# Optimization experiments

Hardware: AMD Instinct MI355X
Metric: run time of the kernel (lower is better)

Reference implementation:

```python
import jax, jax.numpy as jnp
import numpy as np

DIM = 128; DSTATE = 8; DCONV = 4; DTRANK = 8
B = 2; T = 48; H = 16; W = 16
EPS = 1e-5

def _ln(x, w, b):
    mu = jnp.mean(x, -1, keepdims=True)
    var = jnp.mean(jnp.square(x - mu), -1, keepdims=True)
    return (x - mu) * jax.lax.rsqrt(var + EPS) * w + b

def _causal_dwconv(x, w, b):
    # x: [B,L,D], w: [D,K] depthwise, causal padding K-1 on the left
    xt = jnp.transpose(x, (0, 2, 1))  # [B,D,L]
    out = jax.lax.conv_general_dilated(
        xt, w[:, None, :], (1,), [(w.shape[-1] - 1, 0)],
        dimension_numbers=('NCH', 'OIH', 'NCH'),
        feature_group_count=x.shape[-1])
    return jnp.transpose(out + b[:, None], (0, 2, 1))

def _selective_scan(u, dt, A, Bc, Cc, Dp):
    # u, dt: [B,L,D]; A: [D,N]; Bc, Cc: [B,L,N]; Dp: [D]
    dA = jnp.exp(dt[..., None] * A)                          # [B,L,D,N]
    dBx = dt[..., None] * Bc[:, :, None, :] * u[..., None]   # [B,L,D,N]
    def combine(c1, c2):
        a1, b1 = c1; a2, b2 = c2
        return a1 * a2, a2 * b1 + b2
    _, hs = jax.lax.associative_scan(combine, (dA, dBx), axis=1)
    return jnp.einsum('bldn,bln->bld', hs, Cc) + u * Dp

def _bimamba(xn, in_w, conv_w, conv_b, xp_w, dt_w, dt_b, A_log, Dp, out_w):
    # xn: [B,L,DIM]; direction-stacked params have leading axis 2 (fwd/bwd)
    xz = xn @ in_w.T                      # [B,L,2*DIM]
    xh, z = jnp.split(xz, 2, axis=-1)
    acc = 0.0
    for d in range(2):
        xi = xh if d == 0 else xh[:, ::-1]
        zi = z if d == 0 else z[:, ::-1]
        xc = jax.nn.silu(_causal_dwconv(xi, conv_w[d], conv_b[d]))
        proj = xc @ xp_w[d].T             # [B,L,DTRANK+2*DSTATE]
        dtr, Bc, Cc = jnp.split(proj, [DTRANK, DTRANK + DSTATE], axis=-1)
        dt = jax.nn.softplus(dtr @ dt_w[d].T + dt_b[d])
        A = -jnp.exp(A_log[d])
        y = _selective_scan(xc, dt, A, Bc, Cc, Dp[d]) * jax.nn.silu(zi)
        acc = acc + (y if d == 0 else y[:, ::-1])
    return acc @ out_w.T

def setup_inputs():
    key = jax.random.key(0)
    ks = jax.random.split(key, 10)
    s = 0.1
    return {
        "x": jax.random.normal(ks[0], (B, DIM, T, H, W), jnp.float32),
        "norm1_w": jnp.ones((DIM,), jnp.float32),
        "norm1_b": jnp.zeros((DIM,), jnp.float32),
        "norm2_w": jnp.ones((DIM,), jnp.float32),
        "norm2_b": jnp.zeros((DIM,), jnp.float32),
        "subln_w": jnp.ones((DIM,), jnp.float32),
        "subln_b": jnp.zeros((DIM,), jnp.float32),
        "lambda_q": jax.random.normal(ks[1], (DIM,), jnp.float32) * s,
        "in_proj_w": jax.random.normal(ks[2], (2, 2 * DIM, DIM), jnp.float32) * s,
        "conv_w": jax.random.normal(ks[3], (2, 2, DIM, DCONV), jnp.float32) * s,
        "conv_b": jax.random.normal(ks[4], (2, 2, DIM), jnp.float32) * s,
        "x_proj_w": jax.random.normal(ks[5], (2, 2, DTRANK + 2 * DSTATE, DIM), jnp.float32) * s,
        "dt_proj_w": jax.random.normal(ks[6], (2, 2, DIM, DTRANK), jnp.float32) * s,
        "dt_proj_b": jax.random.normal(ks[7], (2, 2, DIM), jnp.float32) * s,
        "A_log": jnp.broadcast_to(jnp.log(jnp.arange(1, DSTATE + 1, dtype=jnp.float32)), (2, 2, DIM, DSTATE)) + 0.0,
        "D": jnp.ones((2, 2, DIM), jnp.float32),
        "out_proj_w": jax.random.normal(ks[8], (2, DIM, DIM), jnp.float32) * s,
    }

def reference(x, norm1_w, norm1_b, norm2_w, norm2_b, subln_w, subln_b,
              lambda_q, in_proj_w, conv_w, conv_b, x_proj_w,
              dt_proj_w, dt_proj_b, A_log, D, out_proj_w):
    Bsz, C = x.shape[0], x.shape[1]
    Tt, Hh, Ww = x.shape[2], x.shape[3], x.shape[4]
    L = Tt * Hh * Ww
    x_flat = jnp.transpose(x.reshape(Bsz, C, L), (0, 2, 1))  # [B,L,C]
    x_norm = _ln(x_flat, norm1_w, norm1_b)
    y1 = _bimamba(x_norm, in_proj_w[0], conv_w[0], conv_b[0], x_proj_w[0],
                  dt_proj_w[0], dt_proj_b[0], A_log[0], D[0], out_proj_w[0])
    y2 = _bimamba(x_norm, in_proj_w[1], conv_w[1], conv_b[1], x_proj_w[1],
                  dt_proj_w[1], dt_proj_b[1], A_log[1], D[1], out_proj_w[1])
    lam = jax.nn.sigmoid(jnp.sum(lambda_q))
    attn = _ln(y1 - lam * y2, subln_w, subln_b)
    out = _ln(x_flat + attn, norm2_w, norm2_b)
    return jnp.transpose(out, (0, 2, 1)).reshape(Bsz, C, Tt, Hh, Ww)
```

## Files before the change

kernel.cpp:

```cpp
#include <hip/hip_runtime.h>
#include <math.h>

#define DIMC 128
#define LSEQ 12288
#define NB 2
#define BLR 24576
#define EPSV 1e-5f
#define NCH 384
#define LC 32
#define KP 132
#define FBP 20

typedef __bf16 bf16x8 __attribute__((ext_vector_type(8)));
typedef __attribute__((ext_vector_type(4))) float f4_t;

__device__ __forceinline__ float sigf(float x){ return 1.f/(1.f+__expf(-x)); }
__device__ __forceinline__ float softplusf(float x){
    return fmaxf(x,0.f) + __logf(1.f + __expf(-fabsf(x)));
}
__device__ __forceinline__ float bf2f(unsigned short u){
    union { unsigned int i; float f; } v; v.i = ((unsigned int)u) << 16; return v.f;
}
__device__ __forceinline__ unsigned short f2bf(float f){
    union { float f; unsigned int i; } v; v.f = f;
    unsigned int b = v.i + 0x7FFFu + ((v.i >> 16) & 1u);
    return (unsigned short)(b >> 16);
}
__device__ __forceinline__ bf16x8 ld_frag8(const unsigned short* p){
    union { uint2 u[2]; bf16x8 v; } r;
    r.u[0] = *(const uint2*)(p);
    r.u[1] = *(const uint2*)(p+4);
    return r.v;
}
__device__ __forceinline__ bf16x8 ld_frag16g(const unsigned short* p){
    union { uint4 u; bf16x8 v; } r; r.u = *(const uint4*)p; return r.v;
}

template<bool FAST>
__device__ __forceinline__ void comp_a8(float dtv, const float* Av, float* a){
    if (FAST){
        float e1 = __expf(dtv*Av[0]);
        float e2 = e1*e1, e4 = e2*e2;
        a[0]=e1; a[1]=e2; a[2]=e2*e1; a[3]=e4;
        a[4]=e4*e1; a[5]=e4*e2; a[6]=a[5]*e1; a[7]=e4*e4;
    } else {
        #pragma unroll
        for (int n = 0; n < 8; n++) a[n] = __expf(dtv*Av[n]);
    }
}

__global__ void k_wall(const float* __restrict__ dtw, const float* __restrict__ xpw,
                       const float* __restrict__ lq,
                       unsigned short* __restrict__ wallb, float* __restrict__ lam){
    int inst = blockIdx.x, j = blockIdx.y, k = threadIdx.x;
    const float* xp = xpw + (size_t)inst*24*128;
    float v;
    if (j < 128){
        const float* dw = dtw + (size_t)inst*128*8 + (size_t)j*8;
        v = 0.f;
        #pragma unroll
        for (int r = 0; r < 8; r++) v += dw[r]*xp[r*128 + k];
    } else {
        v = xp[(8 + (j-128))*128 + k];
    }
    wallb[((size_t)inst*144 + j)*128 + k] = f2bf(v);
    if (inst == 0 && j == 0 && k < 64){
        float s = lq[k] + lq[k+64];
        for (int m = 32; m; m >>= 1) s += __shfl_xor(s, m);
        if (k == 0) *lam = 1.f/(1.f+__expf(-s));
    }
}

__global__ __launch_bounds__(256) void k_prep(const float* __restrict__ wi, const float* __restrict__ ow,
    unsigned short* __restrict__ wib, unsigned short* __restrict__ owb){
    int idx = (blockIdx.x*256 + threadIdx.x)*4;
    const float* src; unsigned short* dst; int off;
    if (idx < 65536){ src = wi;  dst = wib; off = idx; }
    else            { src = ow;  dst = owb; off = idx - 65536; }
    float4 v = *(const float4*)&src[off];
    ushort4 o; o.x=f2bf(v.x); o.y=f2bf(v.y); o.z=f2bf(v.z); o.w=f2bf(v.w);
    *(ushort4*)&dst[off] = o;
}

__global__ __launch_bounds__(256) void k_normT(const float* __restrict__ x,
    const float* __restrict__ w1, const float* __restrict__ b1, unsigned short* __restrict__ xn)
{
    __shared__ float t[64*129];
    __shared__ float red1[256], red2[256];
    __shared__ float stt[128];
    const int bb = blockIdx.x / 192;
    const int l0 = (blockIdx.x % 192) * 64;
    const int tid = threadIdx.x;
    const int li = tid & 63, cg = tid >> 6;
    #pragma unroll
    for (int p = 0; p < 32; p++){
        int c = p*4 + cg;
        t[li*129 + c] = x[(size_t)bb*DIMC*LSEQ + (size_t)c*LSEQ + l0 + li];
    }
    __syncthreads();
    {
        int r = tid >> 2, qg = tid & 3;
        float s = 0.f, s2 = 0.f;
        #pragma unroll
        for (int j = 0; j < 32; j++){ float v = t[r*129 + qg*32 + j]; s += v; s2 += v*v; }
        red1[qg*64 + r] = s; red2[qg*64 + r] = s2;
    }
    __syncthreads();
    if (tid < 64){
        float s = 0.f, s2 = 0.f;
        #pragma unroll
        for (int g = 0; g < 4; g++){ s += red1[g*64 + tid]; s2 += red2[g*64 + tid]; }
        float mu = s*(1.f/128.f);
        float var = s2*(1.f/128.f) - mu*mu;
        stt[tid*2] = mu; stt[tid*2+1] = rsqrtf(var + EPSV);
    }
    __syncthreads();
    const int c2 = (tid & 63)*2, lg = tid >> 6;
    #pragma unroll
    for (int p = 0; p < 16; p++){
        int l = p*4 + lg;
        float mu = stt[l*2], rs = stt[l*2+1];
        float v0 = (t[l*129 + c2    ] - mu)*rs*w1[c2    ] + b1[c2    ];
        float v1 = (t[l*129 + c2 + 1] - mu)*rs*w1[c2 + 1] + b1[c2 + 1];
        unsigned int o = (unsigned int)f2bf(v0) | ((unsigned int)f2bf(v1) << 16);
        *(unsigned int*)&xn[(size_t)(bb*LSEQ + l0 + l)*DIMC + c2] = o;
    }
}

__global__ __launch_bounds__(256,4) void k_inproj(const unsigned short* __restrict__ xn,
    const unsigned short* __restrict__ wib, unsigned short* __restrict__ xz)
{
    __shared__ __align__(16) unsigned short As[64*KP];
    const int row0 = blockIdx.x * 64;
    const int j0   = blockIdx.y * 128;
    const int tid = threadIdx.x;
    const int lane = tid & 63, w = tid >> 6;
    const int m15 = lane & 15, q = lane >> 4;
    const unsigned short* wb = wib + ((size_t)j0 + m15)*DIMC + q*8;
    bf16x8 bc[8], bn[8];
    #pragma unroll
    for (int nt = 0; nt < 8; nt++) bc[nt] = ld_frag16g(wb + nt*2048);
    #pragma unroll
    for (int p = 0; p < 4; p++){
        int idx = p*256 + tid; int li = idx >> 4; int g = (idx & 15)*8;
        uint4 va = *(const uint4*)&xn[(size_t)(row0+li)*DIMC + g];
        *(uint2*)&As[li*KP + g]     = make_uint2(va.x, va.y);
        *(uint2*)&As[li*KP + g + 4] = make_uint2(va.z, va.w);
    }
    __syncthreads();
    f4_t zf = {0.f,0.f,0.f,0.f};
    f4_t acc[8];
    #pragma unroll
    for (int j = 0; j < 8; j++) acc[j] = zf;
    #pragma unroll
    for (int ks = 0; ks < 4; ks++){
        if (ks < 3){
            #pragma unroll
            for (int nt = 0; nt < 8; nt++) bn[nt] = ld_frag16g(wb + nt*2048 + (ks+1)*32);
        }
        bf16x8 a0 = ld_frag8(&As[(w*16 + m15)*KP + ks*32 + q*8]);
        #pragma unroll
        for (int nt = 0; nt < 8; nt++)
            acc[nt] = __builtin_amdgcn_mfma_f32_16x16x32_bf16(a0, bc[nt], acc[nt], 0,0,0);
        #pragma unroll
        for (int nt = 0; nt < 8; nt++) bc[nt] = bn[nt];
    }
    __syncthreads();
    unsigned short* ep = As;
    #pragma unroll
    for (int nt = 0; nt < 8; nt++){
        int row = w*16 + q*4;
        int col = nt*16 + m15;
        #pragma unroll
        for (int i = 0; i < 4; i++)
            ep[(row+i)*KP + col] = f2bf(acc[nt][i]);
    }
    __syncthreads();
    #pragma unroll
    for (int p = 0; p < 4; p++){
        int idx = p*256 + tid; int li = idx >> 4; int g = (idx & 15)*8;
        uint2 u0 = *(const uint2*)&ep[li*KP + g];
        uint2 u1 = *(const uint2*)&ep[li*KP + g + 4];
        uint4 o; o.x=u0.x; o.y=u0.y; o.z=u1.x; o.w=u1.y;
        *(uint4*)&xz[(size_t)(row0+li)*512 + j0 + g] = o;
    }
}

template<bool FAST>
__device__ __forceinline__ void fscan(const unsigned short* __restrict__ As,
    const unsigned short* __restrict__ Ep, const float* __restrict__ fbuf,
    const float* Av, int ch, int d, int dim, float* Ac, float* Bc)
{
    #pragma unroll 8
    for (int s = 0; s < LC; s++){
        int r = ch*32 + (d ? 31-s : s);
        float dtv = bf2f(Ep[r*KP + dim]);
        float uv  = bf2f(As[r*KP + dim]);
        float4 b0 = *(const float4*)&fbuf[r*FBP];
        float4 b1 = *(const float4*)&fbuf[r*FBP + 4];
        float bv[8] = {b0.x,b0.y,b0.z,b0.w,b1.x,b1.y,b1.z,b1.w};
        float du = dtv*uv;
        float a[8];
        comp_a8<FAST>(dtv, Av, a);
        #pragma unroll
        for (int n = 0; n < 8; n++){
            Bc[n] = a[n]*Bc[n] + du*bv[n];
            Ac[n] *= a[n];
        }
    }
}

__global__ __launch_bounds__(256,4) void k_xproj(const unsigned short* __restrict__ xz,
    const unsigned short* __restrict__ wallb, const float* __restrict__ dtb,
    const float* __restrict__ alog, const float* __restrict__ cw, const float* __restrict__ cbv,
    unsigned short* __restrict__ xc, unsigned short* __restrict__ dty,
    float* __restrict__ bcb, float* __restrict__ st)
{
    __shared__ __align__(16) unsigned short As[64*KP];
    __shared__ __align__(16) unsigned short Zb[67*KP];
    __shared__ __align__(16) float fbuf[64*FBP];
    const int row0 = blockIdx.x * 64;
    const int ib   = blockIdx.y;
    const int inst = ib >> 1;
    const int bb   = ib & 1;
    const int m    = inst >> 1;
    const int d    = inst & 1;
    const int tid = threadIdx.x;
    const size_t abase = (size_t)ib * LSEQ * DIMC;
    const int lane = tid & 63, w = tid >> 6;
    const int m15 = lane & 15, q = lane >> 4;
    const unsigned short* wb = wallb + ((size_t)inst*144 + m15)*DIMC + q*8;
    bf16x8 bc[9], bn[9];
    #pragma unroll
    for (int nt = 0; nt < 9; nt++) bc[nt] = ld_frag16g(wb + nt*2048);
    const int start = row0 - (d ? 0 : 3);
    for (int idx = tid; idx < 67*16; idx += 256){
        int r = idx >> 4, cq = idx & 15;
        int l = start + r;
        uint4 v = make_uint4(0,0,0,0);
        if (l >= 0 && l < LSEQ)
            v = *(const uint4*)&xz[((size_t)(bb*LSEQ + l))*512 + m*256 + cq*8];
        *(uint4*)&Zb[r*KP + cq*8] = v;
    }
    __syncthreads();
    {
        const int dimi = tid & 127, lg = tid >> 7;
        float wk[4];
        #pragma unroll
        for (int k = 0; k < 4; k++){
            int kk = d ? 3-k : k;
            wk[k] = cw[((size_t)inst*DIMC + dimi)*4 + kk];
        }
        const float bsv = cbv[inst*DIMC + dimi];
        for (int p = 0; p < 32; p++){
            int li = p*2 + lg;
            float t0 = bf2f(Zb[(li  )*KP + dimi]);
            float t1 = bf2f(Zb[(li+1)*KP + dimi]);
            float t2 = bf2f(Zb[(li+2)*KP + dimi]);
            float t3 = bf2f(Zb[(li+3)*KP + dimi]);
            float v = bsv + wk[0]*t0 + wk[1]*t1 + wk[2]*t2 + wk[3]*t3;
            v = v * sigf(v);
            unsigned short uo = f2bf(v);
            As[li*KP + dimi] = uo;
            xc[abase + (size_t)(row0+li)*DIMC + dimi] = uo;
        }
    }
    __syncthreads();
    f4_t zf = {0.f,0.f,0.f,0.f};
    f4_t acc[9];
    #pragma unroll
    for (int j = 0; j < 9; j++) acc[j] = zf;
    #pragma unroll
    for (int ks = 0; ks < 4; ks++){
        if (ks < 3){
            #pragma unroll
            for (int nt = 0; nt < 9; nt++) bn[nt] = ld_frag16g(wb + nt*2048 + (ks+1)*32);
        }
        bf16x8 a0 = ld_frag8(&As[(w*16 + m15)*KP + ks*32 + q*8]);
        #pragma unroll
        for (int nt = 0; nt < 9; nt++)
            acc[nt] = __builtin_amdgcn_mfma_f32_16x16x32_bf16(a0, bc[nt], acc[nt], 0,0,0);
        #pragma unroll
        for (int nt = 0; nt < 9; nt++) bc[nt] = bn[nt];
    }
    unsigned short* Ep = Zb;
    {
        int row = w*16 + q*4;
        #pragma unroll
        for (int i = 0; i < 4; i++)
            fbuf[(row+i)*FBP + m15] = acc[8][i];
    }
    #pragma unroll
    for (int nt = 0; nt < 8; nt++){
        int col = nt*16 + m15;
        float bias = dtb[inst*DIMC + col];
        int row = w*16 + q*4;
        #pragma unroll
        for (int i = 0; i < 4; i++)
            Ep[(row+i)*KP + col] = f2bf(softplusf(acc[nt][i] + bias));
    }
    __syncthreads();
    {
        int row = tid >> 2, j = (tid & 3)*4;
        float4 v = { fbuf[row*FBP + j], fbuf[row*FBP + j + 1],
                     fbuf[row*FBP + j + 2], fbuf[row*FBP + j + 3] };
        *(float4*)&bcb[((size_t)ib*LSEQ + row0 + row)*16 + j] = v;
    }
    #pragma unroll
    for (int p = 0; p < 4; p++){
        int idx = p*256 + tid; int li = idx >> 4; int g = (idx & 15)*8;
        uint2 u0 = *(const uint2*)&Ep[li*KP + g];
        uint2 u1 = *(const uint2*)&Ep[li*KP + g + 4];
        uint4 o; o.x=u0.x; o.y=u0.y; o.z=u1.x; o.w=u1.y;
        *(uint4*)&dty[abase + (size_t)(row0+li)*DIMC + g] = o;
    }
    const int ch  = tid >> 7;
    const int dim = tid & 127;
    const int bc2 = row0 >> 5;
    const int c   = d ? (NCH-1 - bc2 - ch) : (bc2 + ch);
    float Av[8];
    #pragma unroll
    for (int n = 0; n < 8; n++)
        Av[n] = -__expf(alog[((size_t)inst*DIMC + dim)*8 + n]);
    bool fast = true;
    #pragma unroll
    for (int n = 1; n < 8; n++)
        fast = fast && (fabsf(Av[n] - (float)(n+1)*Av[0]) <= 1e-5f*fabsf(Av[n]));
    float Ac[8], Bc[8];
    #pragma unroll
    for (int n = 0; n < 8; n++){ Ac[n] = 1.f; Bc[n] = 0.f; }
    if (fast) fscan<true >(As, Ep, fbuf, Av, ch, d, dim, Ac, Bc);
    else      fscan<false>(As, Ep, fbuf, Av, ch, d, dim, Ac, Bc);
    float* so = st + (((size_t)ib*NCH + c)*DIMC + dim)*16;
    float4 s0 = {Ac[0],Ac[1],Ac[2],Ac[3]};
    float4 s1 = {Ac[4],Ac[5],Ac[6],Ac[7]};
    float4 s2 = {Bc[0],Bc[1],Bc[2],Bc[3]};
    float4 s3 = {Bc[4],Bc[5],Bc[6],Bc[7]};
    *(float4*)&so[0]  = s0;
    *(float4*)&so[4]  = s1;
    *(float4*)&so[8]  = s2;
    *(float4*)&so[12] = s3;
}

__global__ __launch_bounds__(512) void k_scan2(float* __restrict__ st){
    const int ib   = blockIdx.x >> 7;
    const int dim  = blockIdx.x & 127;
    const int n    = threadIdx.x >> 6;
    const int lane = threadIdx.x & 63;
    const size_t cstride = (size_t)DIMC*16;
    const size_t base = ((size_t)ib*NCH*DIMC + dim)*16 + n;
    float a[6], b[6];
    float Al = 1.f, Bl = 0.f;
    #pragma unroll
    for (int j = 0; j < 6; j++){
        size_t o = base + (size_t)(lane*6 + j)*cstride;
        float A  = st[o];
        float Bv = st[o + 8];
        a[j] = A; b[j] = Bv;
        Bl = A*Bl + Bv;
        Al *= A;
    }
    #pragma unroll
    for (int off = 1; off < 64; off <<= 1){
        float Ao = __shfl_up(Al, off, 64);
        float Bo = __shfl_up(Bl, off, 64);
        if (lane >= off){
            Bl = Al*Bo + Bl;
            Al = Al*Ao;
        }
    }
    float h = __shfl_up(Bl, 1, 64);
    if (lane == 0) h = 0.f;
    #pragma unroll
    for (int j = 0; j < 6; j++){
        size_t o = base + (size_t)(lane*6 + j)*cstride;
        st[o] = h;
        h = a[j]*h + b[j];
    }
}

template<bool FAST>
__device__ __forceinline__ void scan3_body(unsigned short* __restrict__ dty,
    const unsigned short* __restrict__ sdt, const unsigned short* __restrict__ sxc,
    const unsigned short* __restrict__ sz, const float* __restrict__ sbc,
    const float* Av, float Dv, float* h,
    size_t rbase, size_t lbase, int d, int tid)
{
    #pragma unroll 8
    for (int s = 0; s < LC; s++){
        int r = d ? 31-s : s;
        float dtv = bf2f(sdt[r*128 + tid]);
        float uv  = bf2f(sxc[r*128 + tid]);
        float zv  = bf2f(sz [r*128 + tid]);
        float4 bA = *(const float4*)&sbc[r*16];
        float4 bB = *(const float4*)&sbc[r*16 + 4];
        float4 cA = *(const float4*)&sbc[r*16 + 8];
        float4 cB = *(const float4*)&sbc[r*16 + 12];
        float bv[8] = {bA.x,bA.y,bA.z,bA.w,bB.x,bB.y,bB.z,bB.w};
        float cv[8] = {cA.x,cA.y,cA.z,cA.w,cB.x,cB.y,cB.z,cB.w};
        float du = dtv*uv;
        float y = uv*Dv;
        float a[8];
        comp_a8<FAST>(dtv, Av, a);
        #pragma unroll
        for (int n = 0; n < 8; n++){
            h[n] = a[n]*h[n] + du*bv[n];
            y += h[n]*cv[n];
        }
        y *= zv * sigf(zv);
        dty[rbase + (lbase + r)*DIMC + tid] = f2bf(y);
    }
}

__global__ __launch_bounds__(128) void k_scan3(unsigned short* __restrict__ dty,
    const unsigned short* __restrict__ xc, const float* __restrict__ bcb,
    const unsigned short* __restrict__ xz, const float* __restrict__ st,
    const float* __restrict__ alog, const float* __restrict__ dvec)
{
    __shared__ __align__(16) unsigned short sdt[32*128];
    __shared__ __align__(16) unsigned short sxc[32*128];
    __shared__ __align__(16) unsigned short sz [32*128];
    __shared__ __align__(16) float sbc[32*16];
    const int ib = blockIdx.x & 7;
    const int c  = blockIdx.x >> 3;
    const int inst = ib >> 1, bb = ib & 1;
    const int m = inst >> 1, d = inst & 1;
    const int tid = threadIdx.x;
    const size_t rbase = (size_t)ib*LSEQ*DIMC;
    const size_t zbase = (size_t)bb*LSEQ*512 + m*256 + 128;
    const size_t lbase = d ? (size_t)(LSEQ - 32 - c*32) : (size_t)(c*32);
    #pragma unroll
    for (int p = 0; p < 4; p++){
        int idx = p*128 + tid;
        int r = idx >> 4, g = (idx & 15)*8;
        size_t go = rbase + (lbase + r)*DIMC + g;
        *(uint4*)&sdt[r*128 + g] = *(const uint4*)&dty[go];
        *(uint4*)&sxc[r*128 + g] = *(const uint4*)&xc[go];
        *(uint4*)&sz [r*128 + g] = *(const uint4*)&xz[zbase + (lbase + r)*512 + g];
    }
    {
        int r = tid >> 2, j = (tid & 3)*4;
        *(float4*)&sbc[r*16 + j] = *(const float4*)&bcb[((size_t)ib*LSEQ + lbase + r)*16 + j];
    }
    float Av[8];
    #pragma unroll
    for (int n = 0; n < 8; n++)
        Av[n] = -__expf(alog[((size_t)inst*DIMC + tid)*8 + n]);
    bool fast = true;
    #pragma unroll
    for (int n = 1; n < 8; n++)
        fast = fast && (fabsf(Av[n] - (float)(n+1)*Av[0]) <= 1e-5f*fabsf(Av[n]));
    const float Dv = dvec[inst*DIMC + tid];
    float h[8];
    const float* hp = st + (((size_t)ib*NCH + c)*DIMC + tid)*16;
    #pragma unroll
    for (int n = 0; n < 8; n++) h[n] = hp[n];
    __syncthreads();
    if (fast) scan3_body<true >(dty, sdt, sxc, sz, sbc, Av, Dv, h, rbase, lbase, d, tid);
    else      scan3_body<false>(dty, sdt, sxc, sz, sbc, Av, Dv, h, rbase, lbase, d, tid);
}

__global__ __launch_bounds__(256,3) void k_final(const unsigned short* __restrict__ y,
    const unsigned short* __restrict__ owb, const float* __restrict__ x, const float* __restrict__ lamp,
    const float* __restrict__ sw, const float* __restrict__ sb,
    const float* __restrict__ n2w, const float* __restrict__ n2b, float* __restrict__ outp)
{
    __shared__ __align__(16) char smem[52480];
    unsigned short* Ast = (unsigned short*)smem;
    float* yt            = (float*)smem;
    unsigned short* xtb  = (unsigned short*)(smem + 33024);
    float* red1          = (float*)(smem + 49920);
    float* red2          = (float*)(smem + 50944);
    float* stt           = (float*)(smem + 51968);
    const int bb = blockIdx.y;
    const int l0 = blockIdx.x * 64;
    const int tid = threadIdx.x;
    const float lam = *lamp;
    #pragma unroll
    for (int p = 0; p < 8; p++){
        int idx = p*256 + tid; int mm = idx >> 10; int li = (idx >> 4) & 63; int g = (idx & 15)*8;
        uint4 vf = *(const uint4*)&y[(((size_t)(mm*2+0)*NB + bb)*LSEQ + l0 + li)*DIMC + g];
        uint4 vb = *(const uint4*)&y[(((size_t)(mm*2+1)*NB + bb)*LSEQ + l0 + li)*DIMC + g];
        const unsigned short* uf = (const unsigned short*)&vf;
        const unsigned short* ub = (const unsigned short*)&vb;
        unsigned short o[8];
        #pragma unroll
        for (int j = 0; j < 8; j++) o[j] = f2bf(bf2f(uf[j]) + bf2f(ub[j]));
        *(uint2*)&Ast[(mm*64 + li)*KP + g]     = *(uint2*)&o[0];
        *(uint2*)&Ast[(mm*64 + li)*KP + g + 4] = *(uint2*)&o[4];
    }
    __syncthreads();
    const int lane = tid & 63, w = tid >> 6;
    const int m15 = lane & 15, q = lane >> 4;
    f4_t zf = {0.f,0.f,0.f,0.f};
    f4_t acc[2][8];
    #pragma unroll
    for (int i = 0; i < 2; i++)
        #pragma unroll
        for (int j = 0; j < 8; j++) acc[i][j] = zf;
    #pragma unroll
    for (int ks = 0; ks < 4; ks++){
        int k0 = ks*32 + q*8;
        bf16x8 a0 = ld_frag8(&Ast[(       w*16 + m15)*KP + k0]);
        bf16x8 a1 = ld_frag8(&Ast[(64   + w*16 + m15)*KP + k0]);
        #pragma unroll
        for (int nt = 0; nt < 8; nt++){
            bf16x8 b0 = ld_frag16g(&owb[((size_t)0*DIMC + nt*16 + m15)*DIMC + k0]);
            bf16x8 b1 = ld_frag16g(&owb[((size_t)1*DIMC + nt*16 + m15)*DIMC + k0]);
            acc[0][nt] = __builtin_amdgcn_mfma_f32_16x16x32_bf16(a0, b0, acc[0][nt], 0,0,0);
            acc[1][nt] = __builtin_amdgcn_mfma_f32_16x16x32_bf16(a1, b1, acc[1][nt], 0,0,0);
        }
    }
    __syncthreads();
    #pragma unroll
    for (int nt = 0; nt < 8; nt++){
        int row = w*16 + q*4;
        int col = nt*16 + m15;
        #pragma unroll
        for (int i = 0; i < 4; i++)
            yt[(row+i)*129 + col] = acc[0][nt][i] - lam*acc[1][nt][i];
    }
    {
        const int li = tid & 63, cg = tid >> 6;
        #pragma unroll
        for (int p = 0; p < 32; p++){
            int c = p*4 + cg;
            xtb[li*132 + c] = f2bf(x[(size_t)bb*DIMC*LSEQ + (size_t)c*LSEQ + l0 + li]);
        }
    }
    __syncthreads();
    const int r = tid & 63, g = tid >> 6;
    float s = 0.f, s2 = 0.f;
    #pragma unroll
    for (int k = 0; k < 32; k++){ float v = yt[r*129 + g*32 + k]; s += v; s2 += v*v; }
    red1[g*64 + r] = s; red2[g*64 + r] = s2;
    __syncthreads();
    if (tid < 64){
        float ss = 0.f, ss2 = 0.f;
        #pragma unroll
        for (int gg = 0; gg < 4; gg++){ ss += red1[gg*64 + tid]; ss2 += red2[gg*64 + tid]; }
        float mu = ss*(1.f/128.f);
        float var = ss2*(1.f/128.f) - mu*mu;
        stt[tid*2] = mu; stt[tid*2+1] = rsqrtf(var + EPSV);
    }
    __syncthreads();
    float mu1 = stt[r*2], rs1 = stt[r*2+1];
    s = 0.f; s2 = 0.f;
    #pragma unroll
    for (int k = 0; k < 32; k++){
        int c = g*32 + k;
        float v = (yt[r*129+c] - mu1)*rs1*sw[c] + sb[c] + bf2f(xtb[r*132+c]);
        yt[r*129+c] = v;
        s += v; s2 += v*v;
    }
    __syncthreads();
    red1[g*64 + r] = s; red2[g*64 + r] = s2;
    __syncthreads();
    if (tid < 64){
        float ss = 0.f, ss2 = 0.f;
        #pragma unroll
        for (int gg = 0; gg < 4; gg++){ ss += red1[gg*64 + tid]; ss2 += red2[gg*64 + tid]; }
        float mu = ss*(1.f/128.f);
        float var = ss2*(1.f/128.f) - mu*mu;
        stt[tid*2] = mu; stt[tid*2+1] = rsqrtf(var + EPSV);
    }
    __syncthreads();
    float mu2 = stt[r*2], rs2 = stt[r*2+1];
    #pragma unroll
    for (int k = 0; k < 32; k++){
        int c = g*32 + k;
        float o = (yt[r*129+c] - mu2)*rs2*n2w[c] + n2b[c];
        outp[(size_t)bb*DIMC*LSEQ + (size_t)c*LSEQ + l0 + r] = o;
    }
}

extern "C" void kernel_launch(void* const* d_in, const int* in_sizes, int n_in,
                              void* d_out, int out_size, void* d_ws, size_t ws_size,
                              hipStream_t stream)
{
    const float* x    = (const float*)d_in[0];
    const float* n1w  = (const float*)d_in[1];
    const float* n1b  = (const float*)d_in[2];
    const float* n2w  = (const float*)d_in[3];
    const float* n2b  = (const float*)d_in[4];
    const float* slw  = (const float*)d_in[5];
    const float* slb  = (const float*)d_in[6];
    const float* lq   = (const float*)d_in[7];
    const float* wi   = (const float*)d_in[8];
    const float* cw   = (const float*)d_in[9];
    const float* cb   = (const float*)d_in[10];
    const float* xpw  = (const float*)d_in[11];
    const float* dtw  = (const float*)d_in[12];
    const float* dtb  = (const float*)d_in[13];
    const float* alog = (const float*)d_in[14];
    const float* dvec = (const float*)d_in[15];
    const float* ow   = (const float*)d_in[16];

    float* ws = (float*)d_ws;
    unsigned short* xn    = (unsigned short*)(ws);
    unsigned short* xz    = (unsigned short*)(ws + 1572864);
    unsigned short* xc    = (unsigned short*)(ws + 7864320);
    unsigned short* dty   = (unsigned short*)(ws + 14155776);
    float*          bcb   = ws + 20447232;
    float*          st1   = ws + 22020096;
    unsigned short* wallb = (unsigned short*)(ws + 28311552);
    unsigned short* wib   = (unsigned short*)(ws + 28348416);
    unsigned short* owb   = (unsigned short*)(ws + 28381184);
    float*          lam   = ws + 28397568;

    k_wall  <<<dim3(4,144), 128, 0, stream>>>(dtw, xpw, lq, wallb, lam);
    k_prep  <<<96, 256, 0, stream>>>(wi, ow, wib, owb);
    k_normT <<<384, 256, 0, stream>>>(x, n1w, n1b, xn);
    k_inproj<<<dim3(384, 4), 256, 0, stream>>>(xn, wib, xz);
    k_xproj <<<dim3(192, 8), 256, 0, stream>>>(xz, wallb, dtb, alog, cw, cb, xc, dty, bcb, st1);
    k_scan2 <<<1024, 512, 0, stream>>>(st1);
    k_scan3 <<<8*NCH, 128, 0, stream>>>(dty, xc, bcb, xz, st1, alog, dvec);
    k_final <<<dim3(192, 2), 256, 0, stream>>>(dty, owb, x, lam, slw, slb, n2w, n2b, (float*)d_out);
}
```

Baseline: 272.7 us.

## Fuse LayerNorm into in-projection GEMM and compute chunk decay from summed dt

The standalone LayerNorm-transpose kernel is folded into the in-projection kernel. Each block now loads the fp32 input tile, normalizes it in registers and writes bf16 directly into the shared GEMM A-tile, which removes the xn intermediate buffer and one launch. In exchange, the LayerNorm and the strided fp32 input load are repeated for each of the four column blocks in y. Separately, the chunk scan replaces the per-step product of decay factors with a single exp of A times the summed dt. This cuts eight multiplies per step but changes the floating-point rounding slightly.

Measured after the change: 270.6 us. About the same (-0.8%).

```diff
diff --git a/kernel.cpp b/kernel.cpp
--- a/kernel.cpp
+++ b/kernel.cpp
@@ -82,28 +82,40 @@
     *(ushort4*)&dst[off] = o;
 }
 
-__global__ __launch_bounds__(256) void k_normT(const float* __restrict__ x,
-    const float* __restrict__ w1, const float* __restrict__ b1, unsigned short* __restrict__ xn)
+__global__ __launch_bounds__(256,4) void k_inproj(const float* __restrict__ x,
+    const float* __restrict__ w1, const float* __restrict__ b1,
+    const unsigned short* __restrict__ wib, unsigned short* __restrict__ xz)
 {
-    __shared__ float t[64*129];
+    __shared__ __align__(16) float t[64*129];
     __shared__ float red1[256], red2[256];
     __shared__ float stt[128];
+    __shared__ float wln[128], bln[128];
+    unsigned short* As = (unsigned short*)t;
+    const int row0 = blockIdx.x * 64;
     const int bb = blockIdx.x / 192;
     const int l0 = (blockIdx.x % 192) * 64;
+    const int j0 = blockIdx.y * 128;
     const int tid = threadIdx.x;
-    const int li = tid & 63, cg = tid >> 6;
-    #pragma unroll
-    for (int p = 0; p < 32; p++){
-        int c = p*4 + cg;
-        t[li*129 + c] = x[(size_t)bb*DIMC*LSEQ + (size_t)c*LSEQ + l0 + li];
-    }
-    __syncthreads();
-    {
-        int r = tid >> 2, qg = tid & 3;
+    if (tid < 128){ wln[tid] = w1[tid]; bln[tid] = b1[tid]; }
+    {
+        const int li = tid & 63, cg = tid >> 6;
+        #pragma unroll
+        for (int p = 0; p < 32; p++){
+            int c = p*4 + cg;
+            t[li*129 + c] = x[(size_t)bb*DIMC*LSEQ + (size_t)c*LSEQ + l0 + li];
+        }
+    }
+    __syncthreads();
+    const int r4 = tid >> 2, qg = tid & 3;
+    float vals[32];
+    {
         float s = 0.f, s2 = 0.f;
         #pragma unroll
-        for (int j = 0; j < 32; j++){ float v = t[r*129 + qg*32 + j]; s += v; s2 += v*v; }
-        red1[qg*64 + r] = s; red2[qg*64 + r] = s2;
+        for (int j = 0; j < 32; j++){
+            float v = t[r4*129 + qg*32 + j];
+            vals[j] = v; s += v; s2 += v*v;
+        }
+        red1[qg*64 + r4] = s; red2[qg*64 + r4] = s2;
     }
     __syncthreads();
     if (tid < 64){
@@ -115,39 +127,24 @@
         stt[tid*2] = mu; stt[tid*2+1] = rsqrtf(var + EPSV);
     }
     __syncthreads();
-    const int c2 = (tid & 63)*2, lg = tid >> 6;
-    #pragma unroll
-    for (int p = 0; p < 16; p++){
-        int l = p*4 + lg;
-        float mu = stt[l*2], rs = stt[l*2+1];
-        float v0 = (t[l*129 + c2    ] - mu)*rs*w1[c2    ] + b1[c2    ];
-        float v1 = (t[l*129 + c2 + 1] - mu)*rs*w1[c2 + 1] + b1[c2 + 1];
-        unsigned int o = (unsigned int)f2bf(v0) | ((unsigned int)f2bf(v1) << 16);
-        *(unsigned int*)&xn[(size_t)(bb*LSEQ + l0 + l)*DIMC + c2] = o;
-    }
-}
-
-__global__ __launch_bounds__(256,4) void k_inproj(const unsigned short* __restrict__ xn,
-    const unsigned short* __restrict__ wib, unsigned short* __restrict__ xz)
-{
-    __shared__ __align__(16) unsigned short As[64*KP];
-    const int row0 = blockIdx.x * 64;
-    const int j0   = blockIdx.y * 128;
-    const int tid = threadIdx.x;
+    {
+        float mu = stt[r4*2], rs = stt[r4*2+1];
+        #pragma unroll
+        for (int j = 0; j < 32; j += 2){
+            int c = qg*32 + j;
+            float v0 = (vals[j  ]-mu)*rs*wln[c  ] + bln[c  ];
+            float v1 = (vals[j+1]-mu)*rs*wln[c+1] + bln[c+1];
+            unsigned int o = (unsigned int)f2bf(v0) | ((unsigned int)f2bf(v1) << 16);
+            *(unsigned int*)&As[r4*KP + c] = o;
+        }
+    }
+    __syncthreads();
     const int lane = tid & 63, w = tid >> 6;
     const int m15 = lane & 15, q = lane >> 4;
     const unsigned short* wb = wib + ((size_t)j0 + m15)*DIMC + q*8;
     bf16x8 bc[8], bn[8];
     #pragma unroll
     for (int nt = 0; nt < 8; nt++) bc[nt] = ld_frag16g(wb + nt*2048);
-    #pragma unroll
-    for (int p = 0; p < 4; p++){
-        int idx = p*256 + tid; int li = idx >> 4; int g = (idx & 15)*8;
-        uint4 va = *(const uint4*)&xn[(size_t)(row0+li)*DIMC + g];
-        *(uint2*)&As[li*KP + g]     = make_uint2(va.x, va.y);
-        *(uint2*)&As[li*KP + g + 4] = make_uint2(va.z, va.w);
-    }
-    __syncthreads();
     f4_t zf = {0.f,0.f,0.f,0.f};
     f4_t acc[8];
     #pragma unroll
@@ -191,6 +188,7 @@
     const unsigned short* __restrict__ Ep, const float* __restrict__ fbuf,
     const float* Av, int ch, int d, int dim, float* Ac, float* Bc)
 {
+    float dts = 0.f;
     #pragma unroll 8
     for (int s = 0; s < LC; s++){
         int r = ch*32 + (d ? 31-s : s);
@@ -203,11 +201,11 @@
         float a[8];
         comp_a8<FAST>(dtv, Av, a);
         #pragma unroll
-        for (int n = 0; n < 8; n++){
+        for (int n = 0; n < 8; n++)
             Bc[n] = a[n]*Bc[n] + du*bv[n];
-            Ac[n] *= a[n];
-        }
-    }
+        dts += dtv;
+    }
+    comp_a8<FAST>(dts, Av, Ac);
 }
 
 __global__ __launch_bounds__(256,4) void k_xproj(const unsigned short* __restrict__ xz,
@@ -597,7 +595,6 @@
     const float* ow   = (const float*)d_in[16];
 
     float* ws = (float*)d_ws;
-    unsigned short* xn    = (unsigned short*)(ws);
     unsigned short* xz    = (unsigned short*)(ws + 1572864);
     unsigned short* xc    = (unsigned short*)(ws + 7864320);
     unsigned short* dty   = (unsigned short*)(ws + 14155776);
@@ -610,8 +607,7 @@
 
     k_wall  <<<dim3(4,144), 128, 0, stream>>>(dtw, xpw, lq, wallb, lam);
     k_prep  <<<96, 256, 0, stream>>>(wi, ow, wib, owb);
-    k_normT <<<384, 256, 0, stream>>>(x, n1w, n1b, xn);
-    k_inproj<<<dim3(384, 4), 256, 0, stream>>>(xn, wib, xz);
+    k_inproj<<<dim3(384, 4), 256, 0, stream>>>(x, n1w, n1b, wib, xz);
     k_xproj <<<dim3(192, 8), 256, 0, stream>>>(xz, wallb, dtb, alog, cw, cb, xc, dty, bcb, st1);
     k_scan2 <<<1024, 512, 0, stream>>>(st1);
     k_scan3 <<<8*NCH, 128, 0, stream>>>(dty, xc, bcb, xz, st1, alog, dvec);
```
